# Performance work log

Measured on AMD Instinct MI355X. Metric: run time of the kernel, lower is better.

Reference implementation:

```python
import jax, jax.numpy as jnp
import numpy as np

B, S, D = 2, 2048, 2048
HK, HV = 16, 32
DK, DV = 128, 128
KDIM = HK * DK          # 2048
VDIM = HV * DV          # 4096
CONV_DIM = 2 * KDIM + VDIM  # 8192
KSIZE = 4
EPS = 1e-6


def setup_inputs() -> dict:
    key = jax.random.key(0)
    ks = jax.random.split(key, 10)
    w = lambda i, shape, sc=0.02: jax.random.normal(ks[i], shape, jnp.float32) * sc
    return {
        "hidden_states": jax.random.normal(ks[0], (B, S, D), jnp.float32),
        "w_qkv": w(1, (D, CONV_DIM)),
        "w_z": w(2, (D, VDIM)),
        "w_b": w(3, (D, HV)),
        "w_a": w(4, (D, HV)),
        "w_out": w(5, (VDIM, D)),
        "conv_w": w(6, (CONV_DIM, KSIZE), 0.2),   # depthwise conv kernel [C, K]
        "dt_bias": jnp.ones((HV,), jnp.float32),
        "A_log": jnp.log(jax.random.uniform(ks[7], (HV,), jnp.float32, 1e-3, 16.0)),
        "norm_weight": jnp.ones((DV,), jnp.float32),
    }


def _causal_conv1d(x, w):
    # x: [B,S,C], w: [C,K] depthwise; left-pad K-1 zeros -> causal, output len S
    xp = jnp.pad(x, ((0, 0), (KSIZE - 1, 0), (0, 0)))
    lhs = xp.transpose(0, 2, 1)            # [B,C,S+K-1]
    rhs = w[:, None, :]                    # [C,1,K]
    out = jax.lax.conv_general_dilated(lhs, rhs, (1,), 'VALID',
                                       feature_group_count=CONV_DIM)
    return out.transpose(0, 2, 1)          # [B,S,C]


def _l2norm(x, eps=1e-6):
    return x * jax.lax.rsqrt(jnp.sum(x * x, axis=-1, keepdims=True) + eps)


def _gated_delta_rule(q, k, v, g, beta):
    # q,k: [B,S,H,DK]; v: [B,S,H,DV]; g,beta: [B,S,H]
    q = q * (DK ** -0.5)

    def step(St, inp):
        q_t, k_t, v_t, g_t, b_t = inp      # [B,H,dk], [B,H,dk], [B,H,dv], [B,H], [B,H]
        St = St * jnp.exp(g_t)[..., None, None]             # per-head decay
        v_old = jnp.einsum('bhk,bhkv->bhv', k_t, St)        # read memory
        delta = (v_t - v_old) * b_t[..., None]              # delta-rule update
        St = St + k_t[..., None] * delta[:, :, None, :]     # write memory
        o = jnp.einsum('bhk,bhkv->bhv', q_t, St)            # read output
        return St, o

    tr = lambda x: jnp.moveaxis(x, 1, 0)  # seq-major for scan
    S0 = jnp.zeros((q.shape[0], HV, DK, DV), jnp.float32)
    _, out = jax.lax.scan(step, S0, (tr(q), tr(k), tr(v), tr(g), tr(beta)))
    return jnp.moveaxis(out, 0, 1)         # [B,S,H,DV]


def reference(hidden_states, w_qkv, w_z, w_b, w_a, w_out, conv_w,
              dt_bias, A_log, norm_weight):
    Bb, Ss, _ = hidden_states.shape
    mixed = hidden_states @ w_qkv                           # [B,S,CONV_DIM]
    z = (hidden_states @ w_z).reshape(Bb, Ss, HV, DV)
    b = hidden_states @ w_b                                 # [B,S,HV]
    a = hidden_states @ w_a                                 # [B,S,HV]

    mixed = jax.nn.silu(_causal_conv1d(mixed, conv_w))
    q, k, v = jnp.split(mixed, [KDIM, 2 * KDIM], axis=-1)
    q = _l2norm(q.reshape(Bb, Ss, HK, DK))
    k = _l2norm(k.reshape(Bb, Ss, HK, DK))
    v = v.reshape(Bb, Ss, HV, DV)

    beta = jax.nn.sigmoid(b)
    g = -jnp.exp(A_log) * jax.nn.softplus(a + dt_bias)      # [B,S,HV]

    rep = HV // HK
    q = jnp.repeat(q, rep, axis=2)
    k = jnp.repeat(k, rep, axis=2)

    core = _gated_delta_rule(q, k, v, g, beta)              # [B,S,HV,DV]

    # gated RMSNorm over DV: norm(x)*weight*silu(gate)
    var = jnp.mean(core * core, axis=-1, keepdims=True)
    core = core * jax.lax.rsqrt(var + EPS) * norm_weight
    core = core * jax.nn.silu(z)

    return core.reshape(Bb, Ss, VDIM) @ w_out               # [B,S,D]
```

## Files before the change

kernel.cpp:

```cpp
#include <hip/hip_runtime.h>
#include <hip/hip_bf16.h>
#include <cstdint>
#include <cstddef>


typedef __bf16 bf16;
typedef __bf16 bf16x8 __attribute__((ext_vector_type(8)));
typedef __bf16 bf16x4v __attribute__((ext_vector_type(4)));
typedef float f32x4 __attribute__((ext_vector_type(4)));

#define NB 2
#define NS 2048
#define ND 2048
#define NHK 16
#define NHV 32
#define NDK 128
#define NDV 128
#define NKDIM 2048
#define NVDIM 4096
#define NCONV 8192

__device__ __forceinline__ bool detect_f32(const void* dt_raw) {
  return ((const uint32_t*)dt_raw)[0] == 0x3F800000u;
}
__device__ __forceinline__ float inval(const void* p, size_t i, bool f32in) {
  return f32in ? ((const float*)p)[i] : (float)((const bf16*)p)[i];
}

__device__ __forceinline__ void gload_lds16(const bf16* gp, bf16* lp) {
  typedef __attribute__((address_space(1))) const void gvoid_t;
  typedef __attribute__((address_space(3))) void lvoid_t;
  __builtin_amdgcn_global_load_lds((gvoid_t*)gp, (lvoid_t*)lp, 16, 0, 0);
}

typedef __attribute__((address_space(3))) const bf16 lds_cbf16;
__device__ __forceinline__ bf16x8 lds_read16(const bf16* p) {
  bf16x8 r;
  asm volatile("ds_read_b128 %0, %1" : "=v"(r) : "v"((lds_cbf16*)p));
  return r;
}

__global__ __launch_bounds__(256) void convert_hs(const void* __restrict__ in,
    const void* __restrict__ dt_raw, bf16* __restrict__ out)
{
  const bool f32in = detect_f32(dt_raw);
  const size_t base = (size_t)(blockIdx.x * 256 + threadIdx.x) * 8;
  bf16x8 o;
#pragma unroll
  for (int j = 0; j < 8; j++) o[j] = (bf16)inval(in, base + j, f32in);
  *(bf16x8*)(out + base) = o;
}

__global__ __launch_bounds__(256) void convert_small(const void* __restrict__ conv_w,
    const void* __restrict__ dt_bias, const void* __restrict__ A_log,
    const void* __restrict__ norm_w, bf16* __restrict__ conv_wB,
    float* __restrict__ dtf, float* __restrict__ alogf, float* __restrict__ normwf)
{
  const bool f32in = detect_f32(dt_bias);
  const int idx = blockIdx.x * 256 + threadIdx.x;
  if (idx < 32768)      conv_wB[idx] = (bf16)inval(conv_w, idx, f32in);
  else if (idx < 32800) dtf[idx - 32768]   = inval(dt_bias, idx - 32768, f32in);
  else if (idx < 32832) alogf[idx - 32800] = inval(A_log, idx - 32800, f32in);
  else if (idx < 32960) normwf[idx - 32832] = inval(norm_w, idx - 32832, f32in);
}

template <bool F32OUT>
__global__ __launch_bounds__(512, 2) void gemm256(const bf16* __restrict__ A,
    const bf16* __restrict__ Bt, void* __restrict__ Cv, int M, int N, int K)
{
  const int nbx = N >> 8;
  const int nwg = gridDim.x;
  const int cpx = nwg >> 3;
  const int wg = (blockIdx.x & 7) * cpx + (blockIdx.x >> 3);
  const int bm = (wg / nbx) << 8;
  const int bn = (wg % nbx) << 8;

  const int t = threadIdx.x;
  const int wave = t >> 6, lane = t & 63;
  const int wm = wave >> 2, wn = wave & 3;
  const int l15 = lane & 15, quad = lane >> 4;

  __shared__ __attribute__((aligned(16))) bf16 sA[4][8192];
  __shared__ __attribute__((aligned(16))) bf16 sB[4][8192];

  const bf16* gA0 = A  + (size_t)(bm + (wave * 2 + 0) * 16 + l15) * K + quad * 8;
  const bf16* gA1 = A  + (size_t)(bm + (wave * 2 + 1) * 16 + l15) * K + quad * 8;
  const bf16* gB0 = Bt + (size_t)(bn + (wave * 2 + 0) * 16 + l15) * K + quad * 8;
  const bf16* gB1 = Bt + (size_t)(bn + (wave * 2 + 1) * 16 + l15) * K + quad * 8;
  const int sd0 = (wave * 2 + 0) * 512;
  const int sd1 = (wave * 2 + 1) * 512;

  auto STAGE = [&](int kt, int buf) {
    const size_t off = (size_t)kt * 32;
    gload_lds16(gA0 + off, &sA[buf][sd0]);
    gload_lds16(gA1 + off, &sA[buf][sd1]);
    gload_lds16(gB0 + off, &sB[buf][sd0]);
    gload_lds16(gB1 + off, &sB[buf][sd1]);
  };

  f32x4 acc[8][4];
#pragma unroll
  for (int i = 0; i < 8; i++)
#pragma unroll
    for (int j = 0; j < 4; j++)
      acc[i][j] = (f32x4){0.f, 0.f, 0.f, 0.f};

  const int nkt = K >> 5;
  const int frag = quad * 128 + l15 * 8;

  STAGE(0, 0); STAGE(1, 1); STAGE(2, 2);
  asm volatile("s_waitcnt vmcnt(8)" ::: "memory");
  __builtin_amdgcn_s_barrier();
  __builtin_amdgcn_sched_barrier(0);

#pragma unroll 4
  for (int tt = 0; tt < nkt; ++tt) {
    const int cur = tt & 3;

    bf16x8 bfr[4], afr[8];
#pragma unroll
    for (int ni = 0; ni < 4; ni++)
      bfr[ni] = lds_read16(&sB[cur][(wn * 4 + ni) * 512 + frag]);
#pragma unroll
    for (int i = 0; i < 8; i++)
      afr[i] = lds_read16(&sA[cur][(wm * 8 + i) * 512 + frag]);

    if (tt + 3 < nkt) STAGE(tt + 3, (tt + 3) & 3);

    asm volatile("s_waitcnt lgkmcnt(0)" ::: "memory");
    __builtin_amdgcn_sched_barrier(0);

    __builtin_amdgcn_s_setprio(1);
#pragma unroll
    for (int i = 0; i < 8; i++)
#pragma unroll
      for (int ni = 0; ni < 4; ni++)
        acc[i][ni] = __builtin_amdgcn_mfma_f32_16x16x32_bf16(
            afr[i], bfr[ni], acc[i][ni], 0, 0, 0);
    __builtin_amdgcn_s_setprio(0);
    __builtin_amdgcn_sched_barrier(0);

    if (tt < nkt - 3)       asm volatile("s_waitcnt vmcnt(8)" ::: "memory");
    else if (tt == nkt - 3) asm volatile("s_waitcnt vmcnt(4)" ::: "memory");
    else if (tt == nkt - 2) asm volatile("s_waitcnt vmcnt(0)" ::: "memory");
    __builtin_amdgcn_s_barrier();
    __builtin_amdgcn_sched_barrier(0);
  }

#pragma unroll
  for (int mi = 0; mi < 8; mi++)
#pragma unroll
    for (int ni = 0; ni < 4; ni++)
#pragma unroll
      for (int r = 0; r < 4; r++) {
        const int row = bm + wm * 128 + mi * 16 + quad * 4 + r;
        const int col = bn + wn * 64 + ni * 16 + l15;
        if (F32OUT)
          ((float*)Cv)[(size_t)row * N + col] = acc[mi][ni][r];
        else
          ((bf16*)Cv)[(size_t)row * N + col] = (bf16)acc[mi][ni][r];
      }
}

template <bool F32OUT>
__global__ __launch_bounds__(256) void gemm_bt(const bf16* __restrict__ A,
    const bf16* __restrict__ Bt, void* __restrict__ Cv, int M, int N, int K)
{
  __shared__ bf16 As[128 * 32];
  __shared__ bf16 Bs[128 * 32];
  const int tid  = threadIdx.x;
  const int lane = tid & 63;
  const int wave = tid >> 6;
  const int wr = wave >> 1, wc = wave & 1;
  const int l15 = lane & 15, quad = lane >> 4;
  const int bm = blockIdx.y * 128;
  const int bn = blockIdx.x * 128;

  f32x4 acc[4][4];
#pragma unroll
  for (int i = 0; i < 4; i++)
#pragma unroll
    for (int j = 0; j < 4; j++)
      acc[i][j] = (f32x4){0.f, 0.f, 0.f, 0.f};

  const int li0 = wave * 128 + lane;
  const int li1 = li0 + 64;
  const int r0 = li0 >> 2, c0 = (li0 & 3) * 8;
  const int r1 = li1 >> 2, c1 = (li1 & 3) * 8;

  for (int k0 = 0; k0 < K; k0 += 32) {
    gload_lds16(A  + (size_t)(bm + r0) * K + k0 + c0, &As[(wave * 2 + 0) * 512]);
    gload_lds16(A  + (size_t)(bm + r1) * K + k0 + c1, &As[(wave * 2 + 1) * 512]);
    gload_lds16(Bt + (size_t)(bn + r0) * K + k0 + c0, &Bs[(wave * 2 + 0) * 512]);
    gload_lds16(Bt + (size_t)(bn + r1) * K + k0 + c1, &Bs[(wave * 2 + 1) * 512]);
    __syncthreads();
    bf16x8 af[4], bfr[4];
#pragma unroll
    for (int mi = 0; mi < 4; mi++)
      af[mi] = *(const bf16x8*)&As[(wr * 64 + mi * 16 + l15) * 32 + quad * 8];
#pragma unroll
    for (int ni = 0; ni < 4; ni++)
      bfr[ni] = *(const bf16x8*)&Bs[(wc * 64 + ni * 16 + l15) * 32 + quad * 8];
#pragma unroll
    for (int mi = 0; mi < 4; mi++)
#pragma unroll
      for (int ni = 0; ni < 4; ni++)
        acc[mi][ni] = __builtin_amdgcn_mfma_f32_16x16x32_bf16(af[mi], bfr[ni], acc[mi][ni], 0, 0, 0);
    __syncthreads();
  }
#pragma unroll
  for (int mi = 0; mi < 4; mi++)
#pragma unroll
    for (int ni = 0; ni < 4; ni++)
#pragma unroll
      for (int r = 0; r < 4; r++) {
        const int row = bm + wr * 64 + mi * 16 + quad * 4 + r;
        const int col = bn + wc * 64 + ni * 16 + l15;
        if (F32OUT)
          ((float*)Cv)[(size_t)row * N + col] = acc[mi][ni][r];
        else
          ((bf16*)Cv)[(size_t)row * N + col] = (bf16)acc[mi][ni][r];
      }
}

__global__ __launch_bounds__(256) void transpose_k(const void* __restrict__ in,
    const void* __restrict__ dt_raw, bf16* __restrict__ out, int K, int N)
{
  const bool f32in = detect_f32(dt_raw);
  __shared__ bf16 tile[32][33];
  const int n0 = blockIdx.x * 32, k0 = blockIdx.y * 32;
  const int x = threadIdx.x, y0 = threadIdx.y;
#pragma unroll
  for (int i = 0; i < 4; i++) {
    int y = y0 + i * 8;
    tile[y][x] = (bf16)inval(in, (size_t)(k0 + y) * N + n0 + x, f32in);
  }
  __syncthreads();
#pragma unroll
  for (int i = 0; i < 4; i++) {
    int y = y0 + i * 8;
    out[(size_t)(n0 + y) * K + k0 + x] = tile[x][y];
  }
}

__global__ __launch_bounds__(256) void build_wba(const void* __restrict__ w_b,
    const void* __restrict__ w_a, const void* __restrict__ dt_raw,
    bf16* __restrict__ wbaT)
{
  const bool f32in = detect_f32(dt_raw);
  const int idx = blockIdx.x * 256 + threadIdx.x;
  const int n = idx >> 11, k = idx & 2047;
  bf16 v = (bf16)0.f;
  if (n < 32) v = (bf16)inval(w_b, (size_t)k * 32 + n, f32in);
  else if (n < 64) v = (bf16)inval(w_a, (size_t)k * 32 + (n - 32), f32in);
  wbaT[idx] = v;
}

__global__ __launch_bounds__(256) void betag_kernel(const bf16* __restrict__ ba,
    const float* __restrict__ dtf, const float* __restrict__ alogf,
    float* __restrict__ g, float* __restrict__ beta)
{
  const int idx = blockIdx.x * 256 + threadIdx.x;
  const int tok = idx >> 6, j = idx & 63;
  const float d = (float)ba[(size_t)tok * 128 + j];
  if (j < 32) {
    beta[(size_t)tok * 32 + j] = 1.f / (1.f + expf(-d));
  } else {
    const int h = j - 32;
    const float x = d + dtf[h];
    const float sp = (x > 20.f) ? x : log1pf(expf(x));
    g[(size_t)tok * 32 + h] = -expf(alogf[h]) * sp;
  }
}

__global__ __launch_bounds__(256) void conv_kernel(const bf16* __restrict__ mixed,
    const bf16* __restrict__ conv_w, bf16* __restrict__ qhat,
    bf16* __restrict__ khat, bf16* __restrict__ vout)
{
  const int blk = blockIdx.x;
  const int b = blk >> 11, s = blk & 2047;
  const int t = threadIdx.x;
  __shared__ float ssq[512];
  __shared__ float rn[32];
  float vals[4][8];
#pragma unroll
  for (int i = 0; i < 4; i++) {
    const int vg = t + 256 * i;
    const int c = vg * 8;
    const bf16x8* wp = (const bf16x8*)(conv_w + (size_t)c * 4);
    const bf16x8 w0 = wp[0], w1 = wp[1], w2 = wp[2], w3 = wp[3];
    float acc[8] = {0.f, 0.f, 0.f, 0.f, 0.f, 0.f, 0.f, 0.f};
#pragma unroll
    for (int l = 0; l < 4; l++) {
      const int ss = s - 3 + l;
      if (ss >= 0) {
        const bf16x8 x8 = *(const bf16x8*)(mixed + (size_t)(b * 2048 + ss) * NCONV + c);
#pragma unroll
        for (int j = 0; j < 8; j++) {
          const int widx = j * 4 + l;
          const float wv = (widx < 8)  ? (float)w0[widx]
                         : (widx < 16) ? (float)w1[widx - 8]
                         : (widx < 24) ? (float)w2[widx - 16]
                                       : (float)w3[widx - 24];
          acc[j] += (float)x8[j] * wv;
        }
      }
    }
    float lsq = 0.f;
#pragma unroll
    for (int j = 0; j < 8; j++) {
      const float x = acc[j];
      const float y = x / (1.f + expf(-x));
      vals[i][j] = y;
      lsq += y * y;
    }
    if (vg < 512) {
      ssq[vg] = lsq;
    } else {
      bf16x8 o;
#pragma unroll
      for (int j = 0; j < 8; j++) o[j] = (bf16)vals[i][j];
      *(bf16x8*)(vout + (size_t)(b * 2048 + s) * NVDIM + (c - 4096)) = o;
    }
  }
  __syncthreads();
  if (t < 32) {
    float sum = 0.f;
#pragma unroll
    for (int u = 0; u < 16; u++) sum += ssq[t * 16 + u];
    float r = rsqrtf(sum + 1e-6f);
    if (t < 16) r *= 0.08838834764831845f;
    rn[t] = r;
  }
  __syncthreads();
#pragma unroll
  for (int i = 0; i < 2; i++) {
    const int vg = t + 256 * i;
    const float sc = rn[vg >> 4];
    bf16x8 o;
#pragma unroll
    for (int j = 0; j < 8; j++) o[j] = (bf16)(vals[i][j] * sc);
    if (vg < 256)
      *(bf16x8*)(qhat + (size_t)(b * 2048 + s) * NKDIM + vg * 8) = o;
    else
      *(bf16x8*)(khat + (size_t)(b * 2048 + s) * NKDIM + (vg - 256) * 8) = o;
  }
}

__global__ __launch_bounds__(256) void prep_kernel(const bf16* __restrict__ qhat,
    const bf16* __restrict__ khat, bf16* __restrict__ vbuf,
    const float* __restrict__ g, const float* __restrict__ beta,
    bf16* __restrict__ Wg, bf16* __restrict__ Mg, float* __restrict__ egG,
    float* __restrict__ sc2G, float* __restrict__ egTotG)
{
  const int bid = blockIdx.x;
  const int c = bid & 127;
  const int h = (bid >> 7) & 31;
  const int b = bid >> 12;
  const int qh = h >> 1;
  const int s0 = c * 16;
  const int t = threadIdx.x;
  const int wave = t >> 6, lane = t & 63;
  const int l15 = lane & 15, quad = lane >> 4;
  const int sidx = t >> 4, seg = t & 15;

  __shared__ __attribute__((aligned(16))) bf16 pK[16 * 136];
  __shared__ __attribute__((aligned(16))) bf16 pQ[16 * 136];
  __shared__ __attribute__((aligned(16))) bf16 pV[16 * 136];
  __shared__ float sA[16 * 17];
  __shared__ float sGc[16], sEg[16], sBt[16];

  const f32x4 zero4 = (f32x4){0.f, 0.f, 0.f, 0.f};

  {
    const size_t kb = ((size_t)(b * 2048 + s0 + sidx) * NHK + qh) * NDK + seg * 8;
    *(bf16x8*)&pK[sidx * 136 + seg * 8] = *(const bf16x8*)(khat + kb);
    *(bf16x8*)&pQ[sidx * 136 + seg * 8] = *(const bf16x8*)(qhat + kb);
    const size_t vb = ((size_t)(b * 2048 + s0 + sidx) * NHV + h) * NDV + seg * 8;
    *(bf16x8*)&pV[sidx * 136 + seg * 8] = *(const bf16x8*)(vbuf + vb);
  }
  if (wave == 0) {
    float gb_r = 0.f;
    if (lane < 16)      gb_r = g[(size_t)(b * 2048 + s0 + lane) * NHV + h];
    else if (lane < 32) gb_r = beta[(size_t)(b * 2048 + s0 + (lane - 16)) * NHV + h];
    float gc = gb_r;
#pragma unroll
    for (int off = 1; off < 16; off <<= 1) {
      const float n = __shfl_up(gc, off);
      if ((lane & 15) >= off) gc += n;
    }
    const float gtot = __shfl(gc, 15);
    if (lane < 16) {
      sGc[lane] = gc;
      const float e = expf(gc);
      sEg[lane] = e;
      const float s2 = expf(gtot - gc);
      egG[(size_t)bid * 16 + lane] = e;
      sc2G[(size_t)bid * 16 + lane] = s2;
      if (lane == 15) egTotG[bid] = e;
    } else if (lane < 32) {
      sBt[lane - 16] = gb_r;
    }
  }
  __syncthreads();

  f32x4 accKK = zero4, accQK = zero4;
  if (wave == 0) {
#pragma unroll
    for (int kk = 0; kk < 4; kk++) {
      const bf16x8 af = *(const bf16x8*)&pK[l15 * 136 + kk * 32 + quad * 8];
      accKK = __builtin_amdgcn_mfma_f32_16x16x32_bf16(af, af, accKK, 0, 0, 0);
    }
#pragma unroll
    for (int r = 0; r < 4; r++) {
      const int tt = quad * 4 + r, ii = l15;
      float a = 0.f;
      if (ii < tt) a = sBt[tt] * expf(sGc[tt] - sGc[ii]) * accKK[r];
      sA[tt * 17 + ii] = a;
    }
  } else if (wave == 1) {
#pragma unroll
    for (int kk = 0; kk < 4; kk++) {
      const bf16x8 af = *(const bf16x8*)&pQ[l15 * 136 + kk * 32 + quad * 8];
      const bf16x8 bf_ = *(const bf16x8*)&pK[l15 * 136 + kk * 32 + quad * 8];
      accQK = __builtin_amdgcn_mfma_f32_16x16x32_bf16(af, bf_, accQK, 0, 0, 0);
    }
#pragma unroll
    for (int r = 0; r < 4; r++) {
      const int tt = quad * 4 + r, ii = l15;
      const float m = (ii <= tt) ? expf(sGc[tt] - sGc[ii]) * accQK[r] : 0.f;
      Mg[(size_t)bid * 512 + tt * 32 + ii] = (bf16)m;
      Mg[(size_t)bid * 512 + tt * 32 + 16 + ii] = (bf16)0.f;
    }
  }
  __syncthreads();

  {
    const int j = t;
    float x[16];
#pragma unroll
    for (int tt = 0; tt < 16; tt++) {
      float r = (j < 128) ? sBt[tt] * sEg[tt] * (float)pK[tt * 136 + j]
                          : sBt[tt] * (float)pV[tt * 136 + (j - 128)];
#pragma unroll
      for (int i = 0; i < 16; i++)
        if (i < tt) r = fmaf(-sA[tt * 17 + i], x[i], r);
      x[tt] = r;
    }
    if (j < 128) {
#pragma unroll
      for (int tt = 0; tt < 16; tt++)
        Wg[(size_t)bid * 2048 + tt * 128 + j] = (bf16)x[tt];
    } else {
#pragma unroll
      for (int tt = 0; tt < 16; tt++)
        vbuf[((size_t)(b * 2048 + s0 + tt) * NHV + h) * NDV + (j - 128)] = (bf16)x[tt];
    }
  }
}

__global__ __launch_bounds__(256, 2) void core_kernel(const bf16* __restrict__ qhat,
    const bf16* __restrict__ khat, const bf16* __restrict__ Ug,
    const bf16* __restrict__ Wg, const bf16* __restrict__ Mg,
    const float* __restrict__ egG, const float* __restrict__ sc2G,
    const float* __restrict__ egTotG, bf16* __restrict__ corep)
{
  const int bid = blockIdx.x;
  const int vblk = (bid & 7) * 64 + (bid >> 3);
  const int dvc = vblk & 7;
  const int h = (vblk >> 3) & 31;
  const int b = vblk >> 8;
  const int qh = h >> 1;
  const int dvbase = dvc * 16;
  const int t = threadIdx.x;
  const int wave = t >> 6, lane = t & 63;
  const int l15 = lane & 15, quad = lane >> 4;
  const int sidx = t >> 4, seg = t & 15;
  const size_t cb = (size_t)(b * 32 + h) * 128;

  __shared__ __attribute__((aligned(16))) bf16 sKb[2][16 * 136];
  __shared__ __attribute__((aligned(16))) bf16 sKT[128 * 40];
  __shared__ __attribute__((aligned(16))) bf16 sSt[2][16 * 136];
  __shared__ __attribute__((aligned(16))) bf16 sD[16 * 40];
  __shared__ __attribute__((aligned(16))) bf16 sD2[16 * 40];

  const f32x4 zero4 = (f32x4){0.f, 0.f, 0.f, 0.f};
  for (int i = t; i < 272; i += 256) {
    *(f32x4*)&sSt[0][i * 8] = zero4;
    *(f32x4*)&sSt[1][i * 8] = zero4;
  }
  for (int i = t; i < 80; i += 256) {
    *(f32x4*)&sD[i * 8] = zero4;
    *(f32x4*)&sD2[i * 8] = zero4;
  }
  for (int i = t; i < 640; i += 256) *(f32x4*)&sKT[i * 8] = zero4;

  f32x4 accS[2] = {zero4, zero4};

  const int swz = (l15 & 7) << 3;

  bf16x8 kv_r;
  bf16x8 wf[4]; float u4[4], sc2_4[4];
  bf16x8 qf[4], mf; float eg_4[4];
  float egTot_r;

  auto load_kv = [&](int c) {
    const int cc = c < 128 ? c : 127;
    kv_r = *(const bf16x8*)(khat +
        ((size_t)(b * 2048 + cc * 16 + sidx) * NHK + qh) * NDK + seg * 8);
  };
  auto load_w0 = [&](int c) {
    const int cc = c < 128 ? c : 127;
    const size_t wb = (cb + cc) * 2048 + (size_t)l15 * 128 + quad * 8;
#pragma unroll
    for (int kk = 0; kk < 4; kk++) wf[kk] = *(const bf16x8*)(Wg + wb + kk * 32);
#pragma unroll
    for (int r = 0; r < 4; r++) {
      u4[r] = (float)Ug[((size_t)(b * 2048 + cc * 16 + quad * 4 + r) * NHV + h) * NDV
                        + dvbase + l15];
      sc2_4[r] = sc2G[(cb + cc) * 16 + quad * 4 + r];
    }
  };
  auto load_qf = [&](int c) {
    const int cc = c < 128 ? c : 127;
    const size_t qb = ((size_t)(b * 2048 + cc * 16 + l15) * NHK + qh) * NDK + quad * 8;
#pragma unroll
    for (int kk = 0; kk < 4; kk++) qf[kk] = *(const bf16x8*)(qhat + qb + kk * 32);
  };
  auto load_w1m = [&](int c) {
    const int cc = c < 128 ? c : 127;
    mf = *(const bf16x8*)(Mg + (cb + cc) * 512 + l15 * 32 + quad * 8);
#pragma unroll
    for (int r = 0; r < 4; r++) eg_4[r] = egG[(cb + cc) * 16 + quad * 4 + r];
  };
  auto load_egtot = [&](int c) { egTot_r = egTotG[cb + (c < 128 ? c : 127)]; };

  load_kv(0);
  *(bf16x8*)&sKb[0][sidx * 136 + seg * 8] = kv_r;
  load_kv(1);
  if (wave == 0) load_w0(0);
  else if (wave == 1) { load_qf(0); load_w1m(0); }
  load_egtot(0);
  __syncthreads();

#pragma unroll 1
  for (int ch = 0; ch < 128; ++ch) {
    const int cur = ch & 1, nxt = cur ^ 1;
    const int s0 = ch * 16;
    f32x4 accO = zero4;
    if (wave == 0) {
      f32x4 aH = zero4, aL = zero4;
#pragma unroll
      for (int kk = 0; kk < 4; kk++) {
        const int col = (kk * 32 + quad * 8) ^ swz;
        const bf16x8 sh = *(const bf16x8*)&sSt[0][l15 * 136 + col];
        const bf16x8 sl = *(const bf16x8*)&sSt[1][l15 * 136 + col];
        aH = __builtin_amdgcn_mfma_f32_16x16x32_bf16(wf[kk], sh, aH, 0, 0, 0);
        aL = __builtin_amdgcn_mfma_f32_16x16x32_bf16(wf[kk], sl, aL, 0, 0, 0);
      }
      bf16x4v d4, d24;
#pragma unroll
      for (int r = 0; r < 4; r++) {
        const float d = u4[r] - (aH[r] + aL[r]);
        d4[r] = (bf16)d;
        d24[r] = (bf16)(d * sc2_4[r]);
      }
      *(bf16x4v*)&sD[l15 * 40 + quad * 4] = d4;
      *(bf16x4v*)&sD2[l15 * 40 + quad * 4] = d24;
      load_w0(ch + 1);
    } else if (wave == 1) {
      f32x4 aH = zero4, aL = zero4;
#pragma unroll
      for (int kk = 0; kk < 4; kk++) {
        const int col = (kk * 32 + quad * 8) ^ swz;
        const bf16x8 sh = *(const bf16x8*)&sSt[0][l15 * 136 + col];
        const bf16x8 sl = *(const bf16x8*)&sSt[1][l15 * 136 + col];
        aH = __builtin_amdgcn_mfma_f32_16x16x32_bf16(qf[kk], sh, aH, 0, 0, 0);
        aL = __builtin_amdgcn_mfma_f32_16x16x32_bf16(qf[kk], sl, aL, 0, 0, 0);
      }
#pragma unroll
      for (int r = 0; r < 4; r++) accO[r] = eg_4[r] * (aH[r] + aL[r]);
      load_qf(ch + 1);
    } else {
      const int dk_w = (wave - 2) * 64 + lane;
#pragma unroll
      for (int ih = 0; ih < 2; ih++) {
        bf16x8 kt;
#pragma unroll
        for (int j = 0; j < 8; j++) kt[j] = sKb[cur][(ih * 8 + j) * 136 + dk_w];
        *(bf16x8*)&sKT[dk_w * 40 + ih * 8] = kt;
      }
    }
    __syncthreads();
    *(bf16x8*)&sKb[nxt][sidx * 136 + seg * 8] = kv_r;
    load_kv(ch + 2);
    if (wave == 1) {
      const bf16x8 bD = *(const bf16x8*)&sD[l15 * 40 + quad * 8];
      accO = __builtin_amdgcn_mfma_f32_16x16x32_bf16(mf, bD, accO, 0, 0, 0);
#pragma unroll
      for (int r = 0; r < 4; r++)
        corep[((size_t)(b * 2048 + s0 + quad * 4 + r) * NHV + h) * NDV + dvbase + l15]
            = (bf16)accO[r];
      load_w1m(ch + 1);
    }
    {
      const bf16x8 bD2 = *(const bf16x8*)&sD2[l15 * 40 + quad * 8];
#pragma unroll
      for (int ti = 0; ti < 2; ti++) {
        const int dk0 = wave * 32 + ti * 16;
        const bf16x8 kf = *(const bf16x8*)&sKT[(dk0 + l15) * 40 + quad * 8];
        accS[ti] = accS[ti] * egTot_r;
        accS[ti] = __builtin_amdgcn_mfma_f32_16x16x32_bf16(kf, bD2, accS[ti], 0, 0, 0);
      }
      load_egtot(ch + 1);
#pragma unroll
      for (int ti = 0; ti < 2; ti++) {
        const int dk0 = wave * 32 + ti * 16;
        bf16x4v hi4, lo4;
#pragma unroll
        for (int r = 0; r < 4; r++) {
          const float v = accS[ti][r];
          const bf16 hi = (bf16)v;
          hi4[r] = hi;
          lo4[r] = (bf16)(v - (float)hi);
        }
        const int col = (dk0 + quad * 4) ^ swz;
        *(bf16x4v*)&sSt[0][l15 * 136 + col] = hi4;
        *(bf16x4v*)&sSt[1][l15 * 136 + col] = lo4;
      }
    }
    __syncthreads();
  }
}

__global__ __launch_bounds__(128) void normgate_kernel(const bf16* __restrict__ core,
    const bf16* __restrict__ z, const float* __restrict__ normwf,
    bf16* __restrict__ gated)
{
  const size_t idx = blockIdx.x;
  const int t = threadIdx.x;
  const float x = (float)core[idx * 128 + t];
  float p = x * x;
#pragma unroll
  for (int off = 32; off > 0; off >>= 1) p += __shfl_down(p, off);
  __shared__ float s2[2];
  if ((t & 63) == 0) s2[t >> 6] = p;
  __syncthreads();
  const float var = (s2[0] + s2[1]) * (1.f / 128.f);
  const float zv = (float)z[idx * 128 + t];
  const float y = x * rsqrtf(var + 1e-6f) * normwf[t] * (zv / (1.f + expf(-zv)));
  gated[idx * 128 + t] = (bf16)y;
}

extern "C" void kernel_launch(void* const* d_in, const int* in_sizes, int n_in,
                              void* d_out, int out_size, void* d_ws, size_t ws_size,
                              hipStream_t stream)
{
  const void* hs     = d_in[0];
  const void* w_qkv  = d_in[1];
  const void* w_z    = d_in[2];
  const void* w_b    = d_in[3];
  const void* w_a    = d_in[4];
  const void* w_out  = d_in[5];
  const void* conv_w = d_in[6];
  const void* dt_b   = d_in[7];
  const void* A_log  = d_in[8];
  const void* norm_w = d_in[9];

  char* ws = (char*)d_ws;
  bf16*  mixed = (bf16*)(ws + 0);
  bf16*  corep = (bf16*)(ws + 0);
  bf16*  Wg    = (bf16*)(ws + 33554432);
  bf16*  wqkvT = (bf16*)(ws + 67108864);
  bf16*  qhat  = (bf16*)(ws + 67108864);
  bf16*  khat  = (bf16*)(ws + 83886080);
  bf16*  gated = (bf16*)(ws + 67108864);
  bf16*  wzT   = (bf16*)(ws + 100663296);
  bf16*  woutT = (bf16*)(ws + 100663296);
  bf16*  vbuf  = (bf16*)(ws + 117440512);
  bf16*  zbuf  = (bf16*)(ws + 150994944);
  bf16*  hsB   = (bf16*)(ws + 184549376);
  bf16*  Mg    = (bf16*)(ws + 184549376);
  float* egG   = (float*)(ws + 192937984);
  float* sc2G  = (float*)(ws + 193462272);
  float* egTotG= (float*)(ws + 193986560);
  bf16*  wbaT  = (bf16*)(ws + 201326592);
  bf16*  ba    = (bf16*)(ws + 201850880);
  float* gb    = (float*)(ws + 202899456);
  float* betab = (float*)(ws + 203423744);
  bf16*  convwB= (bf16*)(ws + 203948032);
  float* dtf   = (float*)(ws + 204013568);
  float* alogf = (float*)(ws + 204013696);
  float* normwf= (float*)(ws + 204013824);

  convert_hs<<<4096, 256, 0, stream>>>(hs, dt_b, hsB);
  convert_small<<<129, 256, 0, stream>>>(conv_w, dt_b, A_log, norm_w,
                                         convwB, dtf, alogf, normwf);

  const dim3 tb(32, 8);
  transpose_k<<<dim3(NCONV / 32, ND / 32), tb, 0, stream>>>(w_qkv, dt_b, wqkvT, ND, NCONV);
  transpose_k<<<dim3(NVDIM / 32, ND / 32), tb, 0, stream>>>(w_z, dt_b, wzT, ND, NVDIM);
  build_wba<<<1024, 256, 0, stream>>>(w_b, w_a, dt_b, wbaT);

  gemm256<false><<<(NCONV / 256) * (4096 / 256), 512, 0, stream>>>(hsB, wqkvT, mixed, 4096, NCONV, ND);
  gemm256<false><<<(NVDIM / 256) * (4096 / 256), 512, 0, stream>>>(hsB, wzT, zbuf, 4096, NVDIM, ND);
  gemm_bt<false><<<dim3(1, 32), 256, 0, stream>>>(hsB, wbaT, ba, 4096, 128, ND);

  transpose_k<<<dim3(ND / 32, NVDIM / 32), tb, 0, stream>>>(w_out, dt_b, woutT, NVDIM, ND);

  betag_kernel<<<1024, 256, 0, stream>>>(ba, dtf, alogf, gb, betab);
  conv_kernel<<<NB * NS, 256, 0, stream>>>(mixed, convwB, qhat, khat, vbuf);
  prep_kernel<<<8192, 256, 0, stream>>>(qhat, khat, vbuf, gb, betab,
                                        Wg, Mg, egG, sc2G, egTotG);
  core_kernel<<<512, 256, 0, stream>>>(qhat, khat, vbuf, Wg, Mg,
                                       egG, sc2G, egTotG, corep);
  normgate_kernel<<<NB * NS * NHV, 128, 0, stream>>>(corep, zbuf, normwf, gated);

  gemm_bt<true><<<dim3(ND / 128, 32), 256, 0, stream>>>(gated, woutT, (void*)d_out, 4096, ND, NVDIM);
}
```

Before: 864.9 us.

## Add 128x256 triple-buffered GEMM for output projection and reswizzle state LDS layout

Adds a new 512-thread GEMM kernel with 128x256 tiles, a three-stage LDS ring buffer and direct global-to-LDS loads. It replaces the smaller 128x128 gemm_bt used for the final output projection, aiming for more data reuse and better latency hiding. The core recurrent kernel's state buffer in LDS also moves from a padded, XOR-swizzled row layout to a compact fragment-ordered layout with a 2-bit swizzle, to cut bank conflicts and shared memory use. The new GEMM yields only 256 workgroups and needs more LDS per block, so occupancy may be lower.

Measured after the change: 826.0 us. -4.5%, faster.

```diff
diff --git a/kernel.cpp b/kernel.cpp
--- a/kernel.cpp
+++ b/kernel.cpp
@@ -154,6 +154,103 @@
 #pragma unroll
       for (int r = 0; r < 4; r++) {
         const int row = bm + wm * 128 + mi * 16 + quad * 4 + r;
+        const int col = bn + wn * 64 + ni * 16 + l15;
+        if (F32OUT)
+          ((float*)Cv)[(size_t)row * N + col] = acc[mi][ni][r];
+        else
+          ((bf16*)Cv)[(size_t)row * N + col] = (bf16)acc[mi][ni][r];
+      }
+}
+
+template <bool F32OUT>
+__global__ __launch_bounds__(512, 1) void gemm128x256(const bf16* __restrict__ A,
+    const bf16* __restrict__ Bt, void* __restrict__ Cv, int M, int N, int K)
+{
+  const int nbx = N >> 8;
+  const int nwg = gridDim.x;
+  const int cpx = nwg >> 3;
+  const int wg = (blockIdx.x & 7) * cpx + (blockIdx.x >> 3);
+  const int bm = (wg / nbx) << 7;
+  const int bn = (wg % nbx) << 8;
+
+  const int t = threadIdx.x;
+  const int wave = t >> 6, lane = t & 63;
+  const int wm = wave >> 2, wn = wave & 3;
+  const int l15 = lane & 15, quad = lane >> 4;
+
+  __shared__ __attribute__((aligned(16))) bf16 sA[3][4096];
+  __shared__ __attribute__((aligned(16))) bf16 sB[3][8192];
+
+  const bf16* gA0 = A  + (size_t)(bm + wave * 16 + l15) * K + quad * 8;
+  const bf16* gB0 = Bt + (size_t)(bn + (wave * 2 + 0) * 16 + l15) * K + quad * 8;
+  const bf16* gB1 = Bt + (size_t)(bn + (wave * 2 + 1) * 16 + l15) * K + quad * 8;
+  const int sda = wave * 512;
+  const int sd0 = (wave * 2 + 0) * 512;
+  const int sd1 = (wave * 2 + 1) * 512;
+
+  auto STAGE = [&](int kt, int buf) {
+    const size_t off = (size_t)kt * 32;
+    gload_lds16(gA0 + off, &sA[buf][sda]);
+    gload_lds16(gB0 + off, &sB[buf][sd0]);
+    gload_lds16(gB1 + off, &sB[buf][sd1]);
+  };
+
+  f32x4 acc[4][4];
+#pragma unroll
+  for (int i = 0; i < 4; i++)
+#pragma unroll
+    for (int j = 0; j < 4; j++)
+      acc[i][j] = (f32x4){0.f, 0.f, 0.f, 0.f};
+
+  const int nkt = K >> 5;
+  const int frag = quad * 128 + l15 * 8;
+
+  STAGE(0, 0); STAGE(1, 1);
+  asm volatile("s_waitcnt vmcnt(3)" ::: "memory");
+  __builtin_amdgcn_s_barrier();
+  __builtin_amdgcn_sched_barrier(0);
+
+  int cur = 0, sb = 2;
+  for (int tt = 0; tt < nkt; ++tt) {
+    bf16x8 bfr[4], afr[4];
+#pragma unroll
+    for (int ni = 0; ni < 4; ni++)
+      bfr[ni] = lds_read16(&sB[cur][(wn * 4 + ni) * 512 + frag]);
+#pragma unroll
+    for (int i = 0; i < 4; i++)
+      afr[i] = lds_read16(&sA[cur][(wm * 4 + i) * 512 + frag]);
+
+    if (tt + 2 < nkt) STAGE(tt + 2, sb);
+
+    asm volatile("s_waitcnt lgkmcnt(0)" ::: "memory");
+    __builtin_amdgcn_sched_barrier(0);
+
+    __builtin_amdgcn_s_setprio(1);
+#pragma unroll
+    for (int i = 0; i < 4; i++)
+#pragma unroll
+      for (int ni = 0; ni < 4; ni++)
+        acc[i][ni] = __builtin_amdgcn_mfma_f32_16x16x32_bf16(
+            afr[i], bfr[ni], acc[i][ni], 0, 0, 0);
+    __builtin_amdgcn_s_setprio(0);
+    __builtin_amdgcn_sched_barrier(0);
+
+    if (tt < nkt - 2)       asm volatile("s_waitcnt vmcnt(3)" ::: "memory");
+    else if (tt == nkt - 2) asm volatile("s_waitcnt vmcnt(0)" ::: "memory");
+    __builtin_amdgcn_s_barrier();
+    __builtin_amdgcn_sched_barrier(0);
+
+    cur = (cur == 2) ? 0 : cur + 1;
+    sb  = (sb == 2)  ? 0 : sb + 1;
+  }
+
+#pragma unroll
+  for (int mi = 0; mi < 4; mi++)
+#pragma unroll
+    for (int ni = 0; ni < 4; ni++)
+#pragma unroll
+      for (int r = 0; r < 4; r++) {
+        const int row = bm + wm * 64 + mi * 16 + quad * 4 + r;
         const int col = bn + wn * 64 + ni * 16 + l15;
         if (F32OUT)
           ((float*)Cv)[(size_t)row * N + col] = acc[mi][ni][r];
@@ -480,12 +577,12 @@
 
   __shared__ __attribute__((aligned(16))) bf16 sKb[2][16 * 136];
   __shared__ __attribute__((aligned(16))) bf16 sKT[128 * 40];
-  __shared__ __attribute__((aligned(16))) bf16 sSt[2][16 * 136];
+  __shared__ __attribute__((aligned(16))) bf16 sSt[2][2048];
   __shared__ __attribute__((aligned(16))) bf16 sD[16 * 40];
   __shared__ __attribute__((aligned(16))) bf16 sD2[16 * 40];
 
   const f32x4 zero4 = (f32x4){0.f, 0.f, 0.f, 0.f};
-  for (int i = t; i < 272; i += 256) {
+  for (int i = t; i < 256; i += 256) {
     *(f32x4*)&sSt[0][i * 8] = zero4;
     *(f32x4*)&sSt[1][i * 8] = zero4;
   }
@@ -497,7 +594,7 @@
 
   f32x4 accS[2] = {zero4, zero4};
 
-  const int swz = (l15 & 7) << 3;
+  const int swk = l15 & 3;
 
   bf16x8 kv_r;
   bf16x8 wf[4]; float u4[4], sc2_4[4];
@@ -552,9 +649,9 @@
       f32x4 aH = zero4, aL = zero4;
 #pragma unroll
       for (int kk = 0; kk < 4; kk++) {
-        const int col = (kk * 32 + quad * 8) ^ swz;
-        const bf16x8 sh = *(const bf16x8*)&sSt[0][l15 * 136 + col];
-        const bf16x8 sl = *(const bf16x8*)&sSt[1][l15 * 136 + col];
+        const int so = kk * 512 + l15 * 32 + ((kk * 0 + quad) ^ swk) * 8;
+        const bf16x8 sh = *(const bf16x8*)&sSt[0][so];
+        const bf16x8 sl = *(const bf16x8*)&sSt[1][so];
         aH = __builtin_amdgcn_mfma_f32_16x16x32_bf16(wf[kk], sh, aH, 0, 0, 0);
         aL = __builtin_amdgcn_mfma_f32_16x16x32_bf16(wf[kk], sl, aL, 0, 0, 0);
       }
@@ -572,9 +669,9 @@
       f32x4 aH = zero4, aL = zero4;
 #pragma unroll
       for (int kk = 0; kk < 4; kk++) {
-        const int col = (kk * 32 + quad * 8) ^ swz;
-        const bf16x8 sh = *(const bf16x8*)&sSt[0][l15 * 136 + col];
-        const bf16x8 sl = *(const bf16x8*)&sSt[1][l15 * 136 + col];
+        const int so = kk * 512 + l15 * 32 + (quad ^ swk) * 8;
+        const bf16x8 sh = *(const bf16x8*)&sSt[0][so];
+        const bf16x8 sl = *(const bf16x8*)&sSt[1][so];
         aH = __builtin_amdgcn_mfma_f32_16x16x32_bf16(qf[kk], sh, aH, 0, 0, 0);
         aL = __builtin_amdgcn_mfma_f32_16x16x32_bf16(qf[kk], sl, aL, 0, 0, 0);
       }
@@ -615,7 +712,6 @@
       load_egtot(ch + 1);
 #pragma unroll
       for (int ti = 0; ti < 2; ti++) {
-        const int dk0 = wave * 32 + ti * 16;
         bf16x4v hi4, lo4;
 #pragma unroll
         for (int r = 0; r < 4; r++) {
@@ -624,9 +720,10 @@
           hi4[r] = hi;
           lo4[r] = (bf16)(v - (float)hi);
         }
-        const int col = (dk0 + quad * 4) ^ swz;
-        *(bf16x4v*)&sSt[0][l15 * 136 + col] = hi4;
-        *(bf16x4v*)&sSt[1][l15 * 136 + col] = lo4;
+        const int qp = (ti * 2 + (quad >> 1)) ^ swk;
+        const int so = wave * 512 + l15 * 32 + qp * 8 + (quad & 1) * 4;
+        *(bf16x4v*)&sSt[0][so] = hi4;
+        *(bf16x4v*)&sSt[1][so] = lo4;
       }
     }
     __syncthreads();
@@ -716,5 +813,5 @@
                                        egG, sc2G, egTotG, corep);
   normgate_kernel<<<NB * NS * NHV, 128, 0, stream>>>(corep, zbuf, normwf, gated);
 
-  gemm_bt<true><<<dim3(ND / 128, 32), 256, 0, stream>>>(gated, woutT, (void*)d_out, 4096, ND, NVDIM);
-}
+  gemm128x256<true><<<(ND / 256) * (4096 / 128), 512, 0, stream>>>(gated, woutT, (void*)d_out, 4096, ND, NVDIM);
+}
```
